# Performance work log

Hardware: AMD Instinct MI355X
Metric: run time of the kernel (lower is better)

The kernel has to match this reference:

```python
import jax, jax.numpy as jnp
import numpy as np

G, N, E, K, D = 32768, 128, 1024, 32, 3
B = G // 2


def setup_inputs() -> dict:
    key = jax.random.key(0)
    ks = jax.random.split(key, 12)
    x = jax.random.normal(ks[0], (G, N, D), dtype=jnp.float32)
    edge_src = jax.random.randint(ks[1], (G, E), 0, N, dtype=jnp.int32)
    edge_dst = jax.random.randint(ks[2], (G, E), 0, N, dtype=jnp.int32)
    ext_x = jax.random.normal(ks[3], (G, K, D), dtype=jnp.float32)
    # xavier-normal-ish 3x3 params
    s = float(np.sqrt(2.0 / (D + D)))
    W = jax.random.normal(ks[4], (D, D), dtype=jnp.float32) * s
    M = jax.random.normal(ks[5], (D, D), dtype=jnp.float32) * s
    U = jax.random.normal(ks[6], (D, D), dtype=jnp.float32) * s
    V = jax.random.normal(ks[7], (D, D), dtype=jnp.float32) * s
    # link-prediction MLP (Linear(6,3), Linear(3,2))
    W1 = jax.random.uniform(ks[8], (2 * D, D), dtype=jnp.float32, minval=-1, maxval=1) / np.sqrt(2 * D)
    b1 = jnp.zeros((D,), dtype=jnp.float32)
    W2 = jax.random.uniform(ks[9], (D, 2), dtype=jnp.float32, minval=-1, maxval=1) / np.sqrt(D)
    b2 = jnp.zeros((2,), dtype=jnp.float32)
    return {"x": x, "edge_src": edge_src, "edge_dst": edge_dst, "ext_x": ext_x,
            "W": W, "M": M, "U": U, "V": V, "W1": W1, "b1": b1, "W2": W2, "b2": b2}


def _neigh_sum(xg, src, dst):
    # gather source node reps and scatter-add into destination nodes: [N, D]
    return jax.ops.segment_sum(xg[src], dst, num_segments=N)


def reference(x, edge_src, edge_dst, ext_x, W, M, U, V, W1, b1, W2, b2):
    # InternalGraphConvolutionLayer: h = relu(x@W + (sum of neighbour reps)@M)
    agg = jax.vmap(_neigh_sum)(x, edge_src, edge_dst)          # [G, N, D]
    h = jax.nn.relu(jnp.einsum('gnd,de->gne', x, W) +
                    jnp.einsum('gnd,de->gne', agg, M))          # [G, N, D]
    emb = jax.nn.softmax(h.sum(axis=1), axis=-1)                # [G, D]
    # ExternalGraphConvolutionLayer: relu(emb@U + sum_k ext_x@V), softmax
    ext = jax.nn.relu(emb @ U + ext_x.sum(axis=1) @ V)          # [G, D]
    g_emb = jax.nn.softmax(ext, axis=-1)                        # [G, D]
    # LinkPredictionLayer on graph pairs
    e1, e2 = g_emb[:B], g_emb[B:]                               # [B, D] each
    t = jnp.concatenate([e1 * e2, e1 + e2], axis=1)             # [B, 2D]
    hlp = jax.nn.relu(t @ W1 + b1)                              # [B, D]
    out = jax.nn.softmax(hlp @ W2 + b2, axis=-1)                # [B, 2]
    return out
```

## Files before the change

kernel.cpp:

```cpp
#include <hip/hip_runtime.h>

#define NG    32768
#define NN    128
#define NE    1024
#define NK    32
#define NB    (NG / 2)
#define RSTR  17
#define AWDW  (NN * RSTR)

__global__ __launch_bounds__(256, 8) void dcnn_adj_kernel(
    const float* __restrict__ x,
    const int*   __restrict__ esrc,
    const int*   __restrict__ edst,
    const float* __restrict__ extx,
    const float* __restrict__ W,
    const float* __restrict__ M,
    const float* __restrict__ U,
    const float* __restrict__ V,
    const float* __restrict__ W1,
    const float* __restrict__ b1,
    const float* __restrict__ W2,
    const float* __restrict__ b2,
    float* __restrict__ out)
{
    __shared__ unsigned A[2 * AWDW];
    __shared__ float pw[4][6];
    __shared__ float ge[2][3];

    const int t     = threadIdx.x;
    const int w     = t >> 6;
    const int lane  = t & 63;
    const int half  = w & 1;
    const int gslot = w >> 1;
    const int pair  = blockIdx.x;
    const int g     = gslot ? (pair + NB) : pair;

    const int gu = __builtin_amdgcn_readfirstlane(g);
    const float* __restrict__ xg = x + (size_t)gu * (NN * 3);

    const int4* sp = (const int4*)(esrc + (size_t)gu * NE);
    const int4* dp = (const int4*)(edst + (size_t)gu * NE);
    const int ebase = half * 128 + lane;
    const int4 s0 = sp[ebase], s1 = sp[ebase + 64];
    const int4 d0 = dp[ebase], d1 = dp[ebase + 64];

    float er0 = 0.f, er1 = 0.f, er2 = 0.f;
    if (half == 0 && lane < NK) {
        const float* ep = extx + (size_t)gu * (NK * 3) + lane * 3;
        er0 = ep[0]; er1 = ep[1]; er2 = ep[2];
    }

    #pragma unroll
    for (int i = 0; i < 17; ++i) A[i * 256 + t] = 0u;
    __syncthreads();

    unsigned* Aw = &A[gslot * AWDW];
    #define SCAT(SV, DV)                                                    \
        {                                                                   \
            const unsigned off = (unsigned)(size_t)&Aw[(DV) * RSTR + ((SV) >> 3)]; \
            const unsigned val = 1u << (4 * ((SV) & 7));                    \
            asm volatile("ds_add_u32 %0, %1" :: "v"(off), "v"(val) : "memory"); \
        }
    SCAT(s0.x, d0.x) SCAT(s0.y, d0.y) SCAT(s0.z, d0.z) SCAT(s0.w, d0.w)
    SCAT(s1.x, d1.x) SCAT(s1.y, d1.y) SCAT(s1.z, d1.z) SCAT(s1.w, d1.w)
    #undef SCAT

    asm volatile("s_waitcnt lgkmcnt(0)" ::: "memory");
    __syncthreads();

    const int row = half * 64 + lane;
    const int r0  = row * RSTR;
    float ac0 = 0.f, ac1 = 0.f, ac2 = 0.f;

    #pragma unroll
    for (int j = 0; j < 16; ++j) {
        const unsigned da = Aw[r0 + j];
        float q[24];
        *(float4*)&q[0]  = *(const float4*)(xg + j * 24);
        *(float4*)&q[4]  = *(const float4*)(xg + j * 24 + 4);
        *(float4*)&q[8]  = *(const float4*)(xg + j * 24 + 8);
        *(float4*)&q[12] = *(const float4*)(xg + j * 24 + 12);
        *(float4*)&q[16] = *(const float4*)(xg + j * 24 + 16);
        *(float4*)&q[20] = *(const float4*)(xg + j * 24 + 20);
        #pragma unroll
        for (int o = 0; o < 8; ++o) {
            const float ca = (float)((da >> (4 * o)) & 15u);
            ac0 += ca * q[o * 3];
            ac1 += ca * q[o * 3 + 1];
            ac2 += ca * q[o * 3 + 2];
        }
    }

    float h0, h1, h2;
    {
        const float* xr = xg + row * 3;
        const float x0 = xr[0], x1 = xr[1], x2 = xr[2];
        h0 = fmaxf(x0 * W[0] + x1 * W[3] + x2 * W[6] +
                   ac0 * M[0] + ac1 * M[3] + ac2 * M[6], 0.f);
        h1 = fmaxf(x0 * W[1] + x1 * W[4] + x2 * W[7] +
                   ac0 * M[1] + ac1 * M[4] + ac2 * M[7], 0.f);
        h2 = fmaxf(x0 * W[2] + x1 * W[5] + x2 * W[8] +
                   ac0 * M[2] + ac1 * M[5] + ac2 * M[8], 0.f);
    }

    #pragma unroll
    for (int off = 16; off > 0; off >>= 1) {
        h0  += __shfl_xor(h0,  off);
        h1  += __shfl_xor(h1,  off);
        h2  += __shfl_xor(h2,  off);
        er0 += __shfl_xor(er0, off);
        er1 += __shfl_xor(er1, off);
        er2 += __shfl_xor(er2, off);
    }
    #define RL(v) (__uint_as_float(__builtin_amdgcn_readlane(__float_as_uint(v), 0)) + \
                   __uint_as_float(__builtin_amdgcn_readlane(__float_as_uint(v), 32)))
    if (lane == 0) {
        pw[w][0] = RL(h0);  pw[w][1] = RL(h1);  pw[w][2] = RL(h2);
        pw[w][3] = RL(er0); pw[w][4] = RL(er1); pw[w][5] = RL(er2);
    }
    #undef RL

    __syncthreads();

    if (half == 0 && lane == 0) {
        const float H0 = pw[w][0] + pw[w + 1][0];
        const float H1 = pw[w][1] + pw[w + 1][1];
        const float H2 = pw[w][2] + pw[w + 1][2];
        const float E0 = pw[w][3] + pw[w + 1][3];
        const float E1 = pw[w][4] + pw[w + 1][4];
        const float E2 = pw[w][5] + pw[w + 1][5];

        const float mx = fmaxf(H0, fmaxf(H1, H2));
        const float e0 = __expf(H0 - mx), e1 = __expf(H1 - mx), e2 = __expf(H2 - mx);
        const float inv = 1.0f / (e0 + e1 + e2);
        const float emb0 = e0 * inv, emb1 = e1 * inv, emb2 = e2 * inv;

        float ext[3];
        #pragma unroll
        for (int e = 0; e < 3; ++e) {
            const float vv = emb0 * U[e] + emb1 * U[3 + e] + emb2 * U[6 + e]
                           + E0   * V[e] + E1   * V[3 + e] + E2   * V[6 + e];
            ext[e] = fmaxf(vv, 0.f);
        }
        const float mx2 = fmaxf(ext[0], fmaxf(ext[1], ext[2]));
        const float f0 = __expf(ext[0] - mx2), f1 = __expf(ext[1] - mx2), f2 = __expf(ext[2] - mx2);
        const float inv2 = 1.0f / (f0 + f1 + f2);
        ge[gslot][0] = f0 * inv2; ge[gslot][1] = f1 * inv2; ge[gslot][2] = f2 * inv2;
    }

    __syncthreads();

    if (t == 0) {
        float tt[6];
        tt[0] = ge[0][0] * ge[1][0];
        tt[1] = ge[0][1] * ge[1][1];
        tt[2] = ge[0][2] * ge[1][2];
        tt[3] = ge[0][0] + ge[1][0];
        tt[4] = ge[0][1] + ge[1][1];
        tt[5] = ge[0][2] + ge[1][2];

        float hl[3];
        #pragma unroll
        for (int j = 0; j < 3; ++j) {
            float vv = b1[j];
            #pragma unroll
            for (int i = 0; i < 6; ++i) vv += tt[i] * W1[i * 3 + j];
            hl[j] = fmaxf(vv, 0.f);
        }

        const float l0 = b2[0] + hl[0] * W2[0] + hl[1] * W2[2] + hl[2] * W2[4];
        const float l1 = b2[1] + hl[0] * W2[1] + hl[1] * W2[3] + hl[2] * W2[5];
        const float mm = fmaxf(l0, l1);
        const float q0 = __expf(l0 - mm), q1 = __expf(l1 - mm);
        const float qi = 1.0f / (q0 + q1);
        out[(size_t)pair * 2    ] = q0 * qi;
        out[(size_t)pair * 2 + 1] = q1 * qi;
    }
}

extern "C" void kernel_launch(void* const* d_in, const int* in_sizes, int n_in,
                              void* d_out, int out_size, void* d_ws, size_t ws_size,
                              hipStream_t stream) {
    const float* x    = (const float*)d_in[0];
    const int*   esrc = (const int*)  d_in[1];
    const int*   edst = (const int*)  d_in[2];
    const float* extx = (const float*)d_in[3];
    const float* W    = (const float*)d_in[4];
    const float* M    = (const float*)d_in[5];
    const float* U    = (const float*)d_in[6];
    const float* V    = (const float*)d_in[7];
    const float* W1   = (const float*)d_in[8];
    const float* b1   = (const float*)d_in[9];
    const float* W2   = (const float*)d_in[10];
    const float* b2   = (const float*)d_in[11];
    float* out = (float*)d_out;

    dcnn_adj_kernel<<<NB, 256, 0, stream>>>(
        x, esrc, edst, extx, W, M, U, V, W1, b1, W2, b2, out);
}
```

Baseline: 388.5 us.

## Split edge scatter between LDS and global-memory atomics in a persistent kernel

Adds a persistent-block kernel (2048 blocks, each looping over 8 graph pairs) that sends half of each graph's edge scatter to LDS ds_add and the other half to global atomics in a per-block workspace tile. The two nibble-packed count tables are summed when the adjacency rows are read. The aim is to ease LDS atomic contention by running two atomic paths in parallel. In exchange it adds global atomic traffic, a zeroing pass over the workspace, and a full vmcnt wait before the read-back. If the workspace is missing or too small, the launcher falls back to the old kernel.

```diff
diff --git a/kernel.cpp b/kernel.cpp
--- a/kernel.cpp
+++ b/kernel.cpp
@@ -7,20 +7,221 @@
 #define NB    (NG / 2)
 #define RSTR  17
 #define AWDW  (NN * RSTR)
-
-__global__ __launch_bounds__(256, 8) void dcnn_adj_kernel(
+#define PERS  2048
+#define ITERS (NB / PERS)
+#define GTDW  (NN * 16)
+#define GBDW  (2 * GTDW)
+
+__global__ __launch_bounds__(256, 8) void dcnn_split_kernel(
     const float* __restrict__ x,
     const int*   __restrict__ esrc,
     const int*   __restrict__ edst,
     const float* __restrict__ extx,
-    const float* __restrict__ W,
-    const float* __restrict__ M,
-    const float* __restrict__ U,
-    const float* __restrict__ V,
-    const float* __restrict__ W1,
-    const float* __restrict__ b1,
-    const float* __restrict__ W2,
-    const float* __restrict__ b2,
+    const float* __restrict__ W, const float* __restrict__ M,
+    const float* __restrict__ U, const float* __restrict__ V,
+    const float* __restrict__ W1, const float* __restrict__ b1,
+    const float* __restrict__ W2, const float* __restrict__ b2,
+    unsigned* __restrict__ gws,
+    float* __restrict__ out)
+{
+    __shared__ unsigned A[2 * AWDW];
+    __shared__ float pw[4][6];
+    __shared__ float ge[2][3];
+
+    const int t     = threadIdx.x;
+    const int w     = t >> 6;
+    const int lane  = t & 63;
+    const int half  = w & 1;
+    const int gslot = w >> 1;
+
+    unsigned* __restrict__ greg = gws + (size_t)blockIdx.x * GBDW;
+
+    for (int it = 0; it < ITERS; ++it) {
+        const int pair = blockIdx.x + it * PERS;
+        const int g    = gslot ? (pair + NB) : pair;
+
+        const int gu = __builtin_amdgcn_readfirstlane(g);
+        const float* __restrict__ xg = x + (size_t)gu * (NN * 3);
+
+        const int4* sp = (const int4*)(esrc + (size_t)gu * NE);
+        const int4* dp = (const int4*)(edst + (size_t)gu * NE);
+        const int ebase = half * 128 + lane;
+        const int4 s0 = sp[ebase], s1 = sp[ebase + 64];
+        const int4 d0 = dp[ebase], d1 = dp[ebase + 64];
+
+        float er0 = 0.f, er1 = 0.f, er2 = 0.f;
+        if (half == 0 && lane < NK) {
+            const float* ep = extx + (size_t)gu * (NK * 3) + lane * 3;
+            er0 = ep[0]; er1 = ep[1]; er2 = ep[2];
+        }
+
+        #pragma unroll
+        for (int i = 0; i < 17; ++i) A[i * 256 + t] = 0u;
+        {
+            uint4* gz = (uint4*)(greg + t * 16);
+            const uint4 z = make_uint4(0u, 0u, 0u, 0u);
+            gz[0] = z; gz[1] = z; gz[2] = z; gz[3] = z;
+        }
+        __syncthreads();
+
+        unsigned* Aw = &A[gslot * AWDW];
+        #define SCATL(SV, DV)                                                   \
+            {                                                                   \
+                const unsigned off = (unsigned)(size_t)&Aw[(DV) * RSTR + ((SV) >> 3)]; \
+                const unsigned val = 1u << (4 * ((SV) & 7));                    \
+                asm volatile("ds_add_u32 %0, %1" :: "v"(off), "v"(val) : "memory"); \
+            }
+        unsigned* gt = greg + gslot * GTDW;
+        #define SCATG(SV, DV)                                                   \
+            {                                                                   \
+                const unsigned long long ad =                                   \
+                    (unsigned long long)(size_t)(gt + (DV) * 16 + ((SV) >> 3)); \
+                const unsigned val = 1u << (4 * ((SV) & 7));                    \
+                asm volatile("global_atomic_add %0, %1, off" :: "v"(ad), "v"(val) : "memory"); \
+            }
+        SCATL(s0.x, d0.x) SCATG(s1.x, d1.x)
+        SCATL(s0.y, d0.y) SCATG(s1.y, d1.y)
+        SCATL(s0.z, d0.z) SCATG(s1.z, d1.z)
+        SCATL(s0.w, d0.w) SCATG(s1.w, d1.w)
+        #undef SCATL
+        #undef SCATG
+
+        asm volatile("s_waitcnt vmcnt(0) lgkmcnt(0)" ::: "memory");
+        __syncthreads();
+
+        const int row = half * 64 + lane;
+        unsigned gq[16];
+        {
+            const unsigned long long ra =
+                (unsigned long long)(size_t)(gt + row * 16);
+            asm volatile(
+                "global_load_dwordx4 %0, %4, off sc0\n\t"
+                "global_load_dwordx4 %1, %4, off offset:16 sc0\n\t"
+                "global_load_dwordx4 %2, %4, off offset:32 sc0\n\t"
+                "global_load_dwordx4 %3, %4, off offset:48 sc0\n\t"
+                "s_waitcnt vmcnt(0)"
+                : "=v"(*(uint4*)&gq[0]), "=v"(*(uint4*)&gq[4]),
+                  "=v"(*(uint4*)&gq[8]), "=v"(*(uint4*)&gq[12])
+                : "v"(ra) : "memory");
+        }
+        __builtin_amdgcn_sched_barrier(0);
+
+        const int r0 = row * RSTR;
+        float ac0 = 0.f, ac1 = 0.f, ac2 = 0.f;
+        #pragma unroll
+        for (int j = 0; j < 16; ++j) {
+            const unsigned d = Aw[r0 + j] + gq[j];
+            float q[24];
+            *(float4*)&q[0]  = *(const float4*)(xg + j * 24);
+            *(float4*)&q[4]  = *(const float4*)(xg + j * 24 + 4);
+            *(float4*)&q[8]  = *(const float4*)(xg + j * 24 + 8);
+            *(float4*)&q[12] = *(const float4*)(xg + j * 24 + 12);
+            *(float4*)&q[16] = *(const float4*)(xg + j * 24 + 16);
+            *(float4*)&q[20] = *(const float4*)(xg + j * 24 + 20);
+            #pragma unroll
+            for (int o = 0; o < 8; ++o) {
+                const float ca = (float)((d >> (4 * o)) & 15u);
+                ac0 += ca * q[o * 3];
+                ac1 += ca * q[o * 3 + 1];
+                ac2 += ca * q[o * 3 + 2];
+            }
+        }
+
+        float h0, h1, h2;
+        {
+            const float* xr = xg + row * 3;
+            const float x0 = xr[0], x1 = xr[1], x2 = xr[2];
+            h0 = fmaxf(x0 * W[0] + x1 * W[3] + x2 * W[6] +
+                       ac0 * M[0] + ac1 * M[3] + ac2 * M[6], 0.f);
+            h1 = fmaxf(x0 * W[1] + x1 * W[4] + x2 * W[7] +
+                       ac0 * M[1] + ac1 * M[4] + ac2 * M[7], 0.f);
+            h2 = fmaxf(x0 * W[2] + x1 * W[5] + x2 * W[8] +
+                       ac0 * M[2] + ac1 * M[5] + ac2 * M[8], 0.f);
+        }
+
+        #pragma unroll
+        for (int off = 16; off > 0; off >>= 1) {
+            h0  += __shfl_xor(h0,  off);
+            h1  += __shfl_xor(h1,  off);
+            h2  += __shfl_xor(h2,  off);
+            er0 += __shfl_xor(er0, off);
+            er1 += __shfl_xor(er1, off);
+            er2 += __shfl_xor(er2, off);
+        }
+        #define RL(v) (__uint_as_float(__builtin_amdgcn_readlane(__float_as_uint(v), 0)) + \
+                       __uint_as_float(__builtin_amdgcn_readlane(__float_as_uint(v), 32)))
+        if (lane == 0) {
+            pw[w][0] = RL(h0);  pw[w][1] = RL(h1);  pw[w][2] = RL(h2);
+            pw[w][3] = RL(er0); pw[w][4] = RL(er1); pw[w][5] = RL(er2);
+        }
+        #undef RL
+
+        __syncthreads();
+
+        if (half == 0 && lane == 0) {
+            const float H0 = pw[w][0] + pw[w + 1][0];
+            const float H1 = pw[w][1] + pw[w + 1][1];
+            const float H2 = pw[w][2] + pw[w + 1][2];
+            const float E0 = pw[w][3] + pw[w + 1][3];
+            const float E1 = pw[w][4] + pw[w + 1][4];
+            const float E2 = pw[w][5] + pw[w + 1][5];
+
+            const float mx = fmaxf(H0, fmaxf(H1, H2));
+            const float e0 = __expf(H0 - mx), e1 = __expf(H1 - mx), e2 = __expf(H2 - mx);
+            const float inv = 1.0f / (e0 + e1 + e2);
+            const float emb0 = e0 * inv, emb1 = e1 * inv, emb2 = e2 * inv;
+
+            float ext[3];
+            #pragma unroll
+            for (int e = 0; e < 3; ++e) {
+                const float vv = emb0 * U[e] + emb1 * U[3 + e] + emb2 * U[6 + e]
+                               + E0   * V[e] + E1   * V[3 + e] + E2   * V[6 + e];
+                ext[e] = fmaxf(vv, 0.f);
+            }
+            const float mx2 = fmaxf(ext[0], fmaxf(ext[1], ext[2]));
+            const float f0 = __expf(ext[0] - mx2), f1 = __expf(ext[1] - mx2), f2 = __expf(ext[2] - mx2);
+            const float inv2 = 1.0f / (f0 + f1 + f2);
+            ge[gslot][0] = f0 * inv2; ge[gslot][1] = f1 * inv2; ge[gslot][2] = f2 * inv2;
+        }
+
+        __syncthreads();
+
+        if (t == 0) {
+            float tt[6];
+            tt[0] = ge[0][0] * ge[1][0];
+            tt[1] = ge[0][1] * ge[1][1];
+            tt[2] = ge[0][2] * ge[1][2];
+            tt[3] = ge[0][0] + ge[1][0];
+            tt[4] = ge[0][1] + ge[1][1];
+            tt[5] = ge[0][2] + ge[1][2];
+
+            float hl[3];
+            #pragma unroll
+            for (int j = 0; j < 3; ++j) {
+                float vv = b1[j];
+                #pragma unroll
+                for (int i = 0; i < 6; ++i) vv += tt[i] * W1[i * 3 + j];
+                hl[j] = fmaxf(vv, 0.f);
+            }
+
+            const float l0 = b2[0] + hl[0] * W2[0] + hl[1] * W2[2] + hl[2] * W2[4];
+            const float l1 = b2[1] + hl[0] * W2[1] + hl[1] * W2[3] + hl[2] * W2[5];
+            const float mm = fmaxf(l0, l1);
+            const float q0 = __expf(l0 - mm), q1 = __expf(l1 - mm);
+            const float qi = 1.0f / (q0 + q1);
+            out[(size_t)pair * 2    ] = q0 * qi;
+            out[(size_t)pair * 2 + 1] = q1 * qi;
+        }
+    }
+}
+
+__global__ __launch_bounds__(256, 8) void dcnn_adj_kernel(
+    const float* __restrict__ x, const int* __restrict__ esrc,
+    const int* __restrict__ edst, const float* __restrict__ extx,
+    const float* __restrict__ W, const float* __restrict__ M,
+    const float* __restrict__ U, const float* __restrict__ V,
+    const float* __restrict__ W1, const float* __restrict__ b1,
+    const float* __restrict__ W2, const float* __restrict__ b2,
     float* __restrict__ out)
 {
     __shared__ unsigned A[2 * AWDW];
@@ -74,7 +275,7 @@
 
     #pragma unroll
     for (int j = 0; j < 16; ++j) {
-        const unsigned da = Aw[r0 + j];
+        const unsigned d = Aw[r0 + j];
         float q[24];
         *(float4*)&q[0]  = *(const float4*)(xg + j * 24);
         *(float4*)&q[4]  = *(const float4*)(xg + j * 24 + 4);
@@ -84,7 +285,7 @@
         *(float4*)&q[20] = *(const float4*)(xg + j * 24 + 20);
         #pragma unroll
         for (int o = 0; o < 8; ++o) {
-            const float ca = (float)((da >> (4 * o)) & 15u);
+            const float ca = (float)((d >> (4 * o)) & 15u);
             ac0 += ca * q[o * 3];
             ac1 += ca * q[o * 3 + 1];
             ac2 += ca * q[o * 3 + 2];
@@ -195,6 +396,13 @@
     const float* b2   = (const float*)d_in[11];
     float* out = (float*)d_out;
 
-    dcnn_adj_kernel<<<NB, 256, 0, stream>>>(
-        x, esrc, edst, extx, W, M, U, V, W1, b1, W2, b2, out);
+    const size_t need = (size_t)PERS * GBDW * sizeof(unsigned);
+    if (d_ws != nullptr && ws_size >= need) {
+        dcnn_split_kernel<<<PERS, 256, 0, stream>>>(
+            x, esrc, edst, extx, W, M, U, V, W1, b1, W2, b2,
+            (unsigned*)d_ws, out);
+    } else {
+        dcnn_adj_kernel<<<NB, 256, 0, stream>>>(
+            x, esrc, edst, extx, W, M, U, V, W1, b1, W2, b2, out);
+    }
 }
```

Measured after the change: 789.5 us. +103.2%, slower.
